# Optimization experiments

Measured on AMD Instinct MI355X. Metric: run time of the kernel, lower is better.

Reference implementation:

```python
import jax, jax.numpy as jnp
import numpy as np

B, N = 1024, 1024
OBS, ACT, WIDTH = 32, 8, 512

def setup_inputs() -> dict:
    key = jax.random.key(0)
    ks = jax.random.split(key, 8)
    s = 0.02  # small weight scale so 1024 Euler steps stay numerically stable
    return {
        "init_obs": jax.random.normal(ks[0], (B, OBS), jnp.float32),
        "actions": jax.random.normal(ks[1], (B, N, ACT), jnp.float32),
        "W0": jax.random.normal(ks[2], (WIDTH, OBS + ACT), jnp.float32) * s,
        "b0": jnp.zeros((WIDTH,), jnp.float32),
        "W1": jax.random.normal(ks[3], (WIDTH, WIDTH), jnp.float32) * s,
        "b1": jnp.zeros((WIDTH,), jnp.float32),
        "W2": jax.random.normal(ks[4], (WIDTH, WIDTH), jnp.float32) * s,
        "b2": jnp.zeros((WIDTH,), jnp.float32),
        "W3": jax.random.normal(ks[5], (OBS, WIDTH), jnp.float32) * s,
        "b3": jnp.zeros((OBS,), jnp.float32),
        "tau": 1,
    }

def _mlp(x, W0, b0, W1, b1, W2, b2, W3, b3):
    # eqx.nn.MLP with depth=3, activation=leaky_relu (no final activation)
    h = jax.nn.leaky_relu(x @ W0.T + b0)
    h = jax.nn.leaky_relu(h @ W1.T + b1)
    h = jax.nn.leaky_relu(h @ W2.T + b2)
    return h @ W3.T + b3

def reference(init_obs, actions, W0, b0, W1, b1, W2, b2, W3, b3, tau):
    # Fixed-step Euler integration: at step k (t = k*tau), action index = k.
    tauf = jnp.asarray(tau, init_obs.dtype)
    a_t = jnp.swapaxes(actions, 0, 1)  # (N, B, ACT)

    def step(y, a):
        dy = _mlp(jnp.concatenate([y, a], axis=-1), W0, b0, W1, b1, W2, b2, W3, b3)
        y_new = y + tauf * dy
        return y_new, y_new

    _, ys = jax.lax.scan(step, init_obs, a_t)  # ys: (N, B, OBS)
    traj = jnp.concatenate([init_obs[None], ys], axis=0)  # (N+1, B, OBS)
    return jnp.swapaxes(traj, 0, 1)  # (B, N+1, OBS)
```

## Files before the change

kernel.cpp:

```cpp
#include <hip/hip_runtime.h>
#include <hip/hip_bf16.h>
#include <stdint.h>

typedef __bf16 bf16;
typedef __attribute__((ext_vector_type(8))) __bf16 bf16x8;
typedef __attribute__((ext_vector_type(4))) float f32x4;
typedef __attribute__((ext_vector_type(2))) unsigned int u32x2;

#define MFMA_B16(a,b,c) __builtin_amdgcn_mfma_f32_16x16x32_bf16((a),(b),(c),0,0,0)

#define BATCH  1024
#define NSTEPS 1024
#define OBS    32
#define ACTD   8
#define WIDTH  512
#define ROWS   16
#define OUTS   ((NSTEPS+1)*OBS)
#define K0     128

#define W0P_OFF 0
#define W0P_N   (WIDTH*K0)
#define W1_OFF  (W0P_OFF + W0P_N)
#define WBIG_N  (WIDTH*WIDTH)
#define W2_OFF  (W1_OFF + WBIG_N)
#define W3_OFF  (W2_OFF + WBIG_N)
#define W3_N    (OBS*WIDTH)
#define TAU_OFF (W3_OFF + W3_N)
#define MB_OFF  606720
#define MB_N    (64*3*4*2048)
#define FLAG_DW_IDX (((MB_OFF + MB_N)/2) + 64)
#define NFLAG   (64*3*4*16)

#define LBAR() do{ asm volatile("s_waitcnt lgkmcnt(0)" ::: "memory"); \
                   __builtin_amdgcn_s_barrier(); \
                   __builtin_amdgcn_sched_barrier(0); }while(0)
#define FBAR() do{ asm volatile("s_waitcnt vmcnt(0) lgkmcnt(0)" ::: "memory"); \
                   __builtin_amdgcn_s_barrier(); \
                   __builtin_amdgcn_sched_barrier(0); }while(0)

__global__ void setup_kernel(const float* __restrict__ W0, const float* __restrict__ b0r,
                             const float* __restrict__ W1, const float* __restrict__ W2,
                             const float* __restrict__ W3,
                             const int* __restrict__ tau, bf16* __restrict__ wsb){
  int i = blockIdx.x*blockDim.x + threadIdx.x;
  int stride = gridDim.x*blockDim.x;
  for (int idx=i; idx<W0P_N; idx+=stride){
    int r = idx >> 7, c = idx & 127;
    float v = 0.0f;
    if (c < 32)       v = W0[r*40 + c];
    else if (c < 64)  v = W0[r*40 + (c-32)];
    else if (c < 72)  v = W0[r*40 + 32 + (c-64)];
    else if (c == 72) v = b0r[r];
    wsb[W0P_OFF+idx] = (bf16)v;
  }
  for (int idx=i; idx<WBIG_N; idx+=stride) wsb[W1_OFF+idx] = (bf16)W1[idx];
  for (int idx=i; idx<WBIG_N; idx+=stride) wsb[W2_OFF+idx] = (bf16)W2[idx];
  for (int idx=i; idx<W3_N;  idx+=stride) wsb[W3_OFF+idx] = (bf16)W3[idx];
  int* flags = ((int*)wsb) + FLAG_DW_IDX;
  for (int idx=i; idx<NFLAG; idx+=stride) flags[idx] = 0;
  if (i==0){
    int ti = *tau;
    float tf;
    if (ti >= -1000000 && ti <= 1000000) tf = (float)ti;
    else { union {int q; float f;} u; u.q = ti; tf = u.f; }
    *(float*)(wsb + TAU_OFF) = tf;
  }
}

__device__ __forceinline__ float leaky(float v){ return v < 0.0f ? 0.01f*v : v; }

__device__ __forceinline__ uint32_t pk2(float a, float b){
  union { bf16 h; uint16_t u; } ua, ub; ua.h = (bf16)a; ub.h = (bf16)b;
  return (uint32_t)ua.u | ((uint32_t)ub.u << 16);
}

__global__ __launch_bounds__(512, 2)
void ode_kernel(const float* __restrict__ init_obs, const float* __restrict__ actions,
                const float* __restrict__ b1g, const float* __restrict__ b2g,
                const float* __restrict__ b3g,
                bf16* __restrict__ wsrw, float* __restrict__ out){
  const bf16* w0g = wsrw + W0P_OFF;
  const bf16* w1g = wsrw + W1_OFF;
  const bf16* w2g = wsrw + W2_OFF;
  const bf16* w3g = wsrw + W3_OFF;
  unsigned long long* mbq = (unsigned long long*)(wsrw + MB_OFF);
  float* mbf = (float*)(wsrw + MB_OFF);
  int* flags = ((int*)wsrw) + FLAG_DW_IDX;
  const float tauf = *(const float*)(wsrw + TAU_OFF);

  __shared__ alignas(16) bf16 w0s[96*512];
  __shared__ alignas(16) bf16 w3s[8*512];
  __shared__ alignas(16) bf16 hF0[ROWS*WIDTH];
  __shared__ alignas(16) bf16 hF1[ROWS*WIDTH];
  __shared__ alignas(16) bf16 xin[ROWS*K0];
  __shared__ alignas(16) float pr[8][16][20];
  __shared__ float yS[ROWS][OBS];
  __shared__ int sdead;

  const int t    = threadIdx.x;
  const int lane = t & 63;
  const int wave = t >> 6;
  const int fm   = lane & 15;
  const int fk   = lane >> 4;
  const int b    = blockIdx.x;
  const int xcd  = b & 7, slot = b >> 3;
  const int g    = xcd*8 + (slot >> 2);
  const int j    = slot & 3;
  const int gb0  = g * ROWS;
  const int pm0 = (j==0)?1:0, pm1 = (j<2)?2:1, pm2 = (j<3)?3:2;

  const int hbase1 = fm*WIDTH + ((fk*8) ^ (fm*8));
  const int xbase0 = fm*K0    + ((fk*8) ^ (fm*8));
  const int chi    = j*128 + wave*16 + fk*4;

  const f32x4 b1q = *(const f32x4*)&b1g[chi];
  const f32x4 b2q = *(const f32x4*)&b2g[chi];

  bf16x8 w1f[16], w2f[16];
  {
    const bf16* p1 = w1g + (size_t)(j*128 + wave*16 + fm)*WIDTH + fk*8;
    const bf16* p2 = w2g + (size_t)(j*128 + wave*16 + fm)*WIDTH + fk*8;
    #pragma unroll
    for (int kk=0; kk<16; kk++) w1f[kk] = *(const bf16x8*)(p1 + kk*32);
    #pragma unroll
    for (int kk=0; kk<16; kk++) w2f[kk] = *(const bf16x8*)(p2 + kk*32);
  }
  {
    #pragma unroll
    for (int n=0; n<4; n++){
      const bf16* s0 = w0g + (size_t)((wave*4+n)*16 + fm)*K0 + fk*8;
      #pragma unroll
      for (int k=0; k<3; k++){
        bf16x8 v = *(const bf16x8*)(s0 + k*32);
        *(bf16x8*)&w0s[((wave*4+n)*3 + k)*512 + lane*8] = v;
      }
    }
    const int nt_ = wave & 1, q_ = wave >> 1;
    bf16x8 v3 = *(const bf16x8*)(w3g + (size_t)(nt_*16 + fm)*WIDTH + j*128 + q_*32 + fk*8);
    *(bf16x8*)&w3s[wave*512 + lane*8] = v3;
  }

  const int urow = t >> 5, ucol = t & 31;
  const float b3v = b3g[ucol];
  float* const outp = out + (size_t)(gb0 + urow)*OUTS + ucol;
  const int arow = (t >> 3) & 15, acol = t & 7;
  const float* const actp = actions + (size_t)(gb0 + arow)*(NSTEPS*ACTD) + acol;
  const int swU    = (urow & 15) << 3;
  const int xin_yh = urow*K0 + (ucol ^ swU);
  const int xin_yl = urow*K0 + ((ucol + 32) ^ swU);
  const int xin_ac = arow*K0 + ((64 + acol) ^ ((arow & 15) << 3));

  {
    if (t == 0) sdead = 0;
    #pragma unroll
    for (int q=0; q<(ROWS*K0)/512; q++) xin[q*512 + t] = (bf16)0.0f;
    __syncthreads();
    float yv = init_obs[(gb0 + urow)*OBS + ucol];
    yS[urow][ucol] = yv;
    if (j == 0) outp[0] = yv;
    bf16 yh = (bf16)yv;
    xin[xin_yh] = yh;
    xin[xin_yl] = (bf16)(yv - (float)yh);
    if (t < 128) xin[xin_ac] = (bf16)actp[0];
    if (t < 16)  xin[t*K0 + (72 ^ ((t&15)*8))] = (bf16)1.0f;
  }
  __syncthreads();

  #pragma unroll
  for (int kk=0; kk<16; kk++){ asm volatile("" : "+v"(w1f[kk])); }
  #pragma unroll
  for (int kk=0; kk<16; kk++){ asm volatile("" : "+v"(w2f[kk])); }

  #define STORE_OWN01(ACC, BQ, HF, HOP) do{ \
    float r0_ = leaky((ACC)[0] + (BQ)[0]); \
    float r1_ = leaky((ACC)[1] + (BQ)[1]); \
    float r2_ = leaky((ACC)[2] + (BQ)[2]); \
    float r3_ = leaky((ACC)[3] + (BQ)[3]); \
    union { u32x2 v; unsigned long long q; } pu_; \
    pu_.v = (u32x2){ pk2(r0_, r1_), pk2(r2_, r3_) }; \
    *(u32x2*)&HF[fm*WIDTH + (chi ^ (fm*8))] = pu_.v; \
    __hip_atomic_store(mbq + (size_t)((g*3+(HOP))*4 + j)*512 + fm*32 + wave*4 + fk, \
                       pu_.q, __ATOMIC_RELAXED, __HIP_MEMORY_SCOPE_AGENT); \
  }while(0)

  #define SYNC_HOP(HOP, ST1) do{ \
    FBAR(); \
    if (t == 0) __hip_atomic_store(flags + ((g*3+(HOP))*4 + j)*16, (ST1), \
                                   __ATOMIC_RELAXED, __HIP_MEMORY_SCOPE_AGENT); \
    if (wave == 0 && lane < 3){ \
      int pm_ = (lane==0)?pm0:((lane==1)?pm1:pm2); \
      const int* fp_ = flags + ((g*3+(HOP))*4 + pm_)*16; \
      int cnt_ = 0; \
      while (!*(volatile int*)&sdead && \
             __hip_atomic_load(fp_, __ATOMIC_RELAXED, __HIP_MEMORY_SCOPE_AGENT) < (ST1)){ \
        __builtin_amdgcn_s_sleep(1); \
        if (++cnt_ > (1<<20)) { *(volatile int*)&sdead = 1; break; } \
      } \
    } \
    LBAR(); \
  }while(0)

  #define GATHER01(HOP, DST) do{ \
    const int br_ = t >> 5, cg_ = t & 31; \
    const size_t hb_ = (size_t)((g*3+(HOP))*4); \
    unsigned long long v0_ = __hip_atomic_load(mbq + (hb_+pm0)*512 + br_*32 + cg_, \
                                 __ATOMIC_RELAXED, __HIP_MEMORY_SCOPE_AGENT); \
    unsigned long long v1_ = __hip_atomic_load(mbq + (hb_+pm1)*512 + br_*32 + cg_, \
                                 __ATOMIC_RELAXED, __HIP_MEMORY_SCOPE_AGENT); \
    unsigned long long v2_ = __hip_atomic_load(mbq + (hb_+pm2)*512 + br_*32 + cg_, \
                                 __ATOMIC_RELAXED, __HIP_MEMORY_SCOPE_AGENT); \
    *(unsigned long long*)&DST[br_*WIDTH + ((pm0*128 + cg_*4) ^ (br_*8))] = v0_; \
    *(unsigned long long*)&DST[br_*WIDTH + ((pm1*128 + cg_*4) ^ (br_*8))] = v1_; \
    *(unsigned long long*)&DST[br_*WIDTH + ((pm2*128 + cg_*4) ^ (br_*8))] = v2_; \
    LBAR(); \
  }while(0)

  #define L2Q(Q) do{ \
    _Pragma("unroll") \
    for (int kk=(Q)*4; kk<(Q)*4+4; kk++){ \
      bf16x8 bb = *(const bf16x8*)&hF1[hbase1 ^ (kk*32)]; \
      acc2 = MFMA_B16(w2f[kk], bb, acc2); \
    } \
  }while(0)

  #define L2MID() do{ \
    if (wave == 0 && lane < 3){ \
      int pm_ = (lane==0)?pm0:((lane==1)?pm1:pm2); \
      const int* fp_ = flags + ((g*3+0)*4 + pm_)*16; \
      int cnt_ = 0; \
      while (!*(volatile int*)&sdead && \
             __hip_atomic_load(fp_, __ATOMIC_RELAXED, __HIP_MEMORY_SCOPE_AGENT) < st1){ \
        __builtin_amdgcn_s_sleep(1); \
        if (++cnt_ > (1<<20)) { *(volatile int*)&sdead = 1; break; } \
      } \
    } \
    LBAR(); \
    GATHER01(0, hF1); \
  }while(0)

  const f32x4 z4 = {0,0,0,0};

  for (int s=0; s<NSTEPS; ++s){
    const int st1 = s + 1;
    const int sidx = (st1 < NSTEPS) ? st1 : 0;
    float av = actp[(size_t)sidx*ACTD];

    {
      #pragma unroll
      for (int n=0; n<4; n++){
        f32x4 acc = {0,0,0,0};
        #pragma unroll
        for (int k=0; k<3; k++){
          bf16x8 a  = *(const bf16x8*)&w0s[((wave*4+n)*3 + k)*512 + lane*8];
          bf16x8 bb = *(const bf16x8*)&xin[xbase0 ^ (k*32)];
          acc = MFMA_B16(a, bb, acc);
        }
        int ob = (wave*4+n)*16 + fk*4;
        u32x2 pw = { pk2(leaky(acc[0]), leaky(acc[1])),
                     pk2(leaky(acc[2]), leaky(acc[3])) };
        *(u32x2*)&hF0[fm*WIDTH + (ob ^ (fm*8))] = pw;
      }
    }
    LBAR();

    {
      f32x4 acc = {0,0,0,0};
      #pragma unroll
      for (int kk=0; kk<16; kk++){
        bf16x8 bb = *(const bf16x8*)&hF0[hbase1 ^ (kk*32)];
        acc = MFMA_B16(w1f[kk], bb, acc);
      }
      STORE_OWN01(acc, b1q, hF1, 0);
    }
    FBAR();
    if (t == 0) __hip_atomic_store(flags + ((g*3+0)*4 + j)*16, st1,
                                   __ATOMIC_RELAXED, __HIP_MEMORY_SCOPE_AGENT);

    f32x4 acc2 = {0,0,0,0};
    switch (j){
      case 0:  L2Q(0); L2MID(); L2Q(1); L2Q(2); L2Q(3); break;
      case 1:  L2Q(1); L2MID(); L2Q(0); L2Q(2); L2Q(3); break;
      case 2:  L2Q(2); L2MID(); L2Q(0); L2Q(1); L2Q(3); break;
      default: L2Q(3); L2MID(); L2Q(0); L2Q(1); L2Q(2); break;
    }
    {
      u32x2 pw = { pk2(leaky(acc2[0]+b2q[0]), leaky(acc2[1]+b2q[1])),
                   pk2(leaky(acc2[2]+b2q[2]), leaky(acc2[3]+b2q[3])) };
      *(u32x2*)&hF0[fm*WIDTH + (chi ^ (fm*8))] = pw;
    }
    LBAR();

    {
      const int q_ = wave >> 1;
      bf16x8 a  = *(const bf16x8*)&w3s[wave*512 + lane*8];
      bf16x8 bb = *(const bf16x8*)&hF0[fm*WIDTH + ((j*128 + q_*32 + fk*8) ^ (fm*8))];
      f32x4 a3 = MFMA_B16(a, bb, z4);
      *(f32x4*)&pr[wave][fm][fk*4] = a3;
    }
    LBAR();

    float ownv;
    {
      if (t < 128) xin[xin_ac] = (bf16)av;
      const int ntc = ucol >> 4, c15 = ucol & 15;
      ownv = ((pr[ntc][urow][c15] + pr[2+ntc][urow][c15])
              + pr[4+ntc][urow][c15]) + pr[6+ntc][urow][c15];
      __hip_atomic_store(mbf + (size_t)((g*3+2)*4 + j)*1024 + urow*32 + ucol,
                         ownv, __ATOMIC_RELAXED, __HIP_MEMORY_SCOPE_AGENT);
    }
    SYNC_HOP(2, st1);

    {
      float vals[4];
      #pragma unroll
      for (int m=0; m<4; m++){
        if (m == j) vals[m] = ownv;
        else vals[m] = __hip_atomic_load(mbf + (size_t)((g*3+2)*4 + m)*1024 + urow*32 + ucol,
                                         __ATOMIC_RELAXED, __HIP_MEMORY_SCOPE_AGENT);
      }
      float dy = b3v + vals[0] + vals[1] + vals[2] + vals[3];
      float yn = yS[urow][ucol] + tauf * dy;
      yS[urow][ucol] = yn;
      if (j == 0) outp[(size_t)st1*OBS] = yn;
      bf16 yh = (bf16)yn;
      xin[xin_yh] = yh;
      xin[xin_yl] = (bf16)(yn - (float)yh);
    }
    LBAR();
  }
  asm volatile("s_waitcnt vmcnt(0) lgkmcnt(0)" ::: "memory");
}

extern "C" void kernel_launch(void* const* d_in, const int* in_sizes, int n_in,
                              void* d_out, int out_size, void* d_ws, size_t ws_size,
                              hipStream_t stream){
  const float* init_obs = (const float*)d_in[0];
  const float* actions  = (const float*)d_in[1];
  const float* W0 = (const float*)d_in[2];
  const float* b0 = (const float*)d_in[3];
  const float* W1 = (const float*)d_in[4];
  const float* b1 = (const float*)d_in[5];
  const float* W2 = (const float*)d_in[6];
  const float* b2 = (const float*)d_in[7];
  const float* W3 = (const float*)d_in[8];
  const float* b3 = (const float*)d_in[9];
  const int*  tau = (const int*)d_in[10];
  bf16* wsb = (bf16*)d_ws;
  float* out = (float*)d_out;

  hipLaunchKernelGGL(setup_kernel, dim3(512), dim3(256), 0, stream,
                     W0, b0, W1, W2, W3, tau, wsb);
  hipLaunchKernelGGL(ode_kernel, dim3(256), dim3(512), 0, stream,
                     init_obs, actions, b1, b2, b3, wsb, out);
}
```

Before: 4.629 ms.

## Replace flag-based inter-block sync with step-tagged mailbox values polled per thread

Removes the separate flag arrays and the full-barrier-then-flag handshake between the four cooperating blocks. Each exchanged value now carries the step number in its upper 32 bits, so consumers poll the data words directly until the tags match. This drops a vmcnt-draining barrier and a flag round trip per hop, which should cut cross-block latency. In exchange each payload doubles in size, every thread spins on global loads, and the mailbox region must be zeroed in setup.

```diff
diff --git a/kernel.cpp b/kernel.cpp
--- a/kernel.cpp
+++ b/kernel.cpp
@@ -6,6 +6,7 @@
 typedef __attribute__((ext_vector_type(8))) __bf16 bf16x8;
 typedef __attribute__((ext_vector_type(4))) float f32x4;
 typedef __attribute__((ext_vector_type(2))) unsigned int u32x2;
+typedef unsigned long long u64;
 
 #define MFMA_B16(a,b,c) __builtin_amdgcn_mfma_f32_16x16x32_bf16((a),(b),(c),0,0,0)
 
@@ -26,15 +27,14 @@
 #define W3_OFF  (W2_OFF + WBIG_N)
 #define W3_N    (OBS*WIDTH)
 #define TAU_OFF (W3_OFF + W3_N)
-#define MB_OFF  606720
-#define MB_N    (64*3*4*2048)
-#define FLAG_DW_IDX (((MB_OFF + MB_N)/2) + 64)
-#define NFLAG   (64*3*4*16)
+#define MB_OFF      606720
+#define DY_U64_BASE 262144
+#define MB_U64_N    393216
+
+#define AL(P)   __hip_atomic_load((P),  __ATOMIC_RELAXED, __HIP_MEMORY_SCOPE_AGENT)
+#define AS(P,V) __hip_atomic_store((P), (V), __ATOMIC_RELAXED, __HIP_MEMORY_SCOPE_AGENT)
 
 #define LBAR() do{ asm volatile("s_waitcnt lgkmcnt(0)" ::: "memory"); \
-                   __builtin_amdgcn_s_barrier(); \
-                   __builtin_amdgcn_sched_barrier(0); }while(0)
-#define FBAR() do{ asm volatile("s_waitcnt vmcnt(0) lgkmcnt(0)" ::: "memory"); \
                    __builtin_amdgcn_s_barrier(); \
                    __builtin_amdgcn_sched_barrier(0); }while(0)
 
@@ -56,8 +56,8 @@
   for (int idx=i; idx<WBIG_N; idx+=stride) wsb[W1_OFF+idx] = (bf16)W1[idx];
   for (int idx=i; idx<WBIG_N; idx+=stride) wsb[W2_OFF+idx] = (bf16)W2[idx];
   for (int idx=i; idx<W3_N;  idx+=stride) wsb[W3_OFF+idx] = (bf16)W3[idx];
-  int* flags = ((int*)wsb) + FLAG_DW_IDX;
-  for (int idx=i; idx<NFLAG; idx+=stride) flags[idx] = 0;
+  u64* mbq = (u64*)(wsb + MB_OFF);
+  for (int idx=i; idx<MB_U64_N; idx+=stride) mbq[idx] = 0ull;
   if (i==0){
     int ti = *tau;
     float tf;
@@ -83,9 +83,7 @@
   const bf16* w1g = wsrw + W1_OFF;
   const bf16* w2g = wsrw + W2_OFF;
   const bf16* w3g = wsrw + W3_OFF;
-  unsigned long long* mbq = (unsigned long long*)(wsrw + MB_OFF);
-  float* mbf = (float*)(wsrw + MB_OFF);
-  int* flags = ((int*)wsrw) + FLAG_DW_IDX;
+  u64* mbq = (u64*)(wsrw + MB_OFF);
   const float tauf = *(const float*)(wsrw + TAU_OFF);
 
   __shared__ alignas(16) bf16 w0s[96*512];
@@ -171,71 +169,12 @@
   #pragma unroll
   for (int kk=0; kk<16; kk++){ asm volatile("" : "+v"(w2f[kk])); }
 
-  #define STORE_OWN01(ACC, BQ, HF, HOP) do{ \
-    float r0_ = leaky((ACC)[0] + (BQ)[0]); \
-    float r1_ = leaky((ACC)[1] + (BQ)[1]); \
-    float r2_ = leaky((ACC)[2] + (BQ)[2]); \
-    float r3_ = leaky((ACC)[3] + (BQ)[3]); \
-    union { u32x2 v; unsigned long long q; } pu_; \
-    pu_.v = (u32x2){ pk2(r0_, r1_), pk2(r2_, r3_) }; \
-    *(u32x2*)&HF[fm*WIDTH + (chi ^ (fm*8))] = pu_.v; \
-    __hip_atomic_store(mbq + (size_t)((g*3+(HOP))*4 + j)*512 + fm*32 + wave*4 + fk, \
-                       pu_.q, __ATOMIC_RELAXED, __HIP_MEMORY_SCOPE_AGENT); \
-  }while(0)
-
-  #define SYNC_HOP(HOP, ST1) do{ \
-    FBAR(); \
-    if (t == 0) __hip_atomic_store(flags + ((g*3+(HOP))*4 + j)*16, (ST1), \
-                                   __ATOMIC_RELAXED, __HIP_MEMORY_SCOPE_AGENT); \
-    if (wave == 0 && lane < 3){ \
-      int pm_ = (lane==0)?pm0:((lane==1)?pm1:pm2); \
-      const int* fp_ = flags + ((g*3+(HOP))*4 + pm_)*16; \
-      int cnt_ = 0; \
-      while (!*(volatile int*)&sdead && \
-             __hip_atomic_load(fp_, __ATOMIC_RELAXED, __HIP_MEMORY_SCOPE_AGENT) < (ST1)){ \
-        __builtin_amdgcn_s_sleep(1); \
-        if (++cnt_ > (1<<20)) { *(volatile int*)&sdead = 1; break; } \
-      } \
-    } \
-    LBAR(); \
-  }while(0)
-
-  #define GATHER01(HOP, DST) do{ \
-    const int br_ = t >> 5, cg_ = t & 31; \
-    const size_t hb_ = (size_t)((g*3+(HOP))*4); \
-    unsigned long long v0_ = __hip_atomic_load(mbq + (hb_+pm0)*512 + br_*32 + cg_, \
-                                 __ATOMIC_RELAXED, __HIP_MEMORY_SCOPE_AGENT); \
-    unsigned long long v1_ = __hip_atomic_load(mbq + (hb_+pm1)*512 + br_*32 + cg_, \
-                                 __ATOMIC_RELAXED, __HIP_MEMORY_SCOPE_AGENT); \
-    unsigned long long v2_ = __hip_atomic_load(mbq + (hb_+pm2)*512 + br_*32 + cg_, \
-                                 __ATOMIC_RELAXED, __HIP_MEMORY_SCOPE_AGENT); \
-    *(unsigned long long*)&DST[br_*WIDTH + ((pm0*128 + cg_*4) ^ (br_*8))] = v0_; \
-    *(unsigned long long*)&DST[br_*WIDTH + ((pm1*128 + cg_*4) ^ (br_*8))] = v1_; \
-    *(unsigned long long*)&DST[br_*WIDTH + ((pm2*128 + cg_*4) ^ (br_*8))] = v2_; \
-    LBAR(); \
-  }while(0)
-
   #define L2Q(Q) do{ \
     _Pragma("unroll") \
     for (int kk=(Q)*4; kk<(Q)*4+4; kk++){ \
-      bf16x8 bb = *(const bf16x8*)&hF1[hbase1 ^ (kk*32)]; \
-      acc2 = MFMA_B16(w2f[kk], bb, acc2); \
+      bf16x8 bb_ = *(const bf16x8*)&hF1[hbase1 ^ (kk*32)]; \
+      acc2 = MFMA_B16(w2f[kk], bb_, acc2); \
     } \
-  }while(0)
-
-  #define L2MID() do{ \
-    if (wave == 0 && lane < 3){ \
-      int pm_ = (lane==0)?pm0:((lane==1)?pm1:pm2); \
-      const int* fp_ = flags + ((g*3+0)*4 + pm_)*16; \
-      int cnt_ = 0; \
-      while (!*(volatile int*)&sdead && \
-             __hip_atomic_load(fp_, __ATOMIC_RELAXED, __HIP_MEMORY_SCOPE_AGENT) < st1){ \
-        __builtin_amdgcn_s_sleep(1); \
-        if (++cnt_ > (1<<20)) { *(volatile int*)&sdead = 1; break; } \
-      } \
-    } \
-    LBAR(); \
-    GATHER01(0, hF1); \
   }while(0)
 
   const f32x4 z4 = {0,0,0,0};
@@ -270,19 +209,51 @@
         bf16x8 bb = *(const bf16x8*)&hF0[hbase1 ^ (kk*32)];
         acc = MFMA_B16(w1f[kk], bb, acc);
       }
-      STORE_OWN01(acc, b1q, hF1, 0);
-    }
-    FBAR();
-    if (t == 0) __hip_atomic_store(flags + ((g*3+0)*4 + j)*16, st1,
-                                   __ATOMIC_RELAXED, __HIP_MEMORY_SCOPE_AGENT);
+      unsigned lo0 = pk2(leaky(acc[0]+b1q[0]), leaky(acc[1]+b1q[1]));
+      unsigned lo1 = pk2(leaky(acc[2]+b1q[2]), leaky(acc[3]+b1q[3]));
+      *(u64*)&hF1[fm*WIDTH + (chi ^ (fm*8))] = (u64)lo0 | ((u64)lo1 << 32);
+      u64 tg = ((u64)(unsigned)st1) << 32;
+      size_t mb = (size_t)(g*4 + j)*1024 + (size_t)(fm*32 + wave*4 + fk)*2;
+      AS(mbq + mb,     (u64)lo0 | tg);
+      AS(mbq + mb + 1, (u64)lo1 | tg);
+    }
+    LBAR();
 
     f32x4 acc2 = {0,0,0,0};
+    {
+      const int br = t >> 5, cg = t & 31;
+      const size_t hb = (size_t)(g*4);
+      const size_t ia = (hb+pm0)*1024 + (size_t)(br*32+cg)*2;
+      const size_t ib = (hb+pm1)*1024 + (size_t)(br*32+cg)*2;
+      const size_t ic = (hb+pm2)*1024 + (size_t)(br*32+cg)*2;
+      u64 a0 = AL(mbq+ia), a1 = AL(mbq+ia+1);
+      u64 b0 = AL(mbq+ib), b1 = AL(mbq+ib+1);
+      u64 c0 = AL(mbq+ic), c1 = AL(mbq+ic+1);
+      switch (j){ case 0: L2Q(0); break; case 1: L2Q(1); break;
+                  case 2: L2Q(2); break; default: L2Q(3); break; }
+      const unsigned sU = (unsigned)st1;
+      int cnt = 0;
+      while (!(((unsigned)(a0>>32)==sU) & ((unsigned)(a1>>32)==sU) &
+               ((unsigned)(b0>>32)==sU) & ((unsigned)(b1>>32)==sU) &
+               ((unsigned)(c0>>32)==sU) & ((unsigned)(c1>>32)==sU))){
+        if (*(volatile int*)&sdead) break;
+        __builtin_amdgcn_s_sleep(2);
+        if (++cnt > (1<<16)) { *(volatile int*)&sdead = 1; break; }
+        a0 = AL(mbq+ia); a1 = AL(mbq+ia+1);
+        b0 = AL(mbq+ib); b1 = AL(mbq+ib+1);
+        c0 = AL(mbq+ic); c1 = AL(mbq+ic+1);
+      }
+      const int sw = br << 3;
+      *(u64*)&hF1[br*WIDTH + ((pm0*128 + cg*4) ^ sw)] = (u64)(unsigned)a0 | ((u64)(unsigned)a1 << 32);
+      *(u64*)&hF1[br*WIDTH + ((pm1*128 + cg*4) ^ sw)] = (u64)(unsigned)b0 | ((u64)(unsigned)b1 << 32);
+      *(u64*)&hF1[br*WIDTH + ((pm2*128 + cg*4) ^ sw)] = (u64)(unsigned)c0 | ((u64)(unsigned)c1 << 32);
+    }
+    LBAR();
     switch (j){
-      case 0:  L2Q(0); L2MID(); L2Q(1); L2Q(2); L2Q(3); break;
-      case 1:  L2Q(1); L2MID(); L2Q(0); L2Q(2); L2Q(3); break;
-      case 2:  L2Q(2); L2MID(); L2Q(0); L2Q(1); L2Q(3); break;
-      default: L2Q(3); L2MID(); L2Q(0); L2Q(1); L2Q(2); break;
-    }
+      case 0:  L2Q(1); L2Q(2); L2Q(3); break;
+      case 1:  L2Q(0); L2Q(2); L2Q(3); break;
+      case 2:  L2Q(0); L2Q(1); L2Q(3); break;
+      default: L2Q(0); L2Q(1); L2Q(2); break; }
     {
       u32x2 pw = { pk2(leaky(acc2[0]+b2q[0]), leaky(acc2[1]+b2q[1])),
                    pk2(leaky(acc2[2]+b2q[2]), leaky(acc2[3]+b2q[3])) };
@@ -305,20 +276,34 @@
       const int ntc = ucol >> 4, c15 = ucol & 15;
       ownv = ((pr[ntc][urow][c15] + pr[2+ntc][urow][c15])
               + pr[4+ntc][urow][c15]) + pr[6+ntc][urow][c15];
-      __hip_atomic_store(mbf + (size_t)((g*3+2)*4 + j)*1024 + urow*32 + ucol,
-                         ownv, __ATOMIC_RELAXED, __HIP_MEMORY_SCOPE_AGENT);
-    }
-    SYNC_HOP(2, st1);
-
-    {
-      float vals[4];
-      #pragma unroll
-      for (int m=0; m<4; m++){
-        if (m == j) vals[m] = ownv;
-        else vals[m] = __hip_atomic_load(mbf + (size_t)((g*3+2)*4 + m)*1024 + urow*32 + ucol,
-                                         __ATOMIC_RELAXED, __HIP_MEMORY_SCOPE_AGENT);
-      }
-      float dy = b3v + vals[0] + vals[1] + vals[2] + vals[3];
+      AS(mbq + DY_U64_BASE + (size_t)(g*4 + j)*512 + urow*32 + ucol,
+         (u64)__float_as_uint(ownv) | (((u64)(unsigned)st1) << 32));
+    }
+
+    {
+      const size_t db = DY_U64_BASE + (size_t)(g*4)*512 + (size_t)(urow*32 + ucol);
+      u64 va = AL(mbq + db + (size_t)pm0*512);
+      u64 vb = AL(mbq + db + (size_t)pm1*512);
+      u64 vc = AL(mbq + db + (size_t)pm2*512);
+      const unsigned sU = (unsigned)st1;
+      int cnt = 0;
+      while (!(((unsigned)(va>>32)==sU) & ((unsigned)(vb>>32)==sU) &
+               ((unsigned)(vc>>32)==sU))){
+        if (*(volatile int*)&sdead) break;
+        __builtin_amdgcn_s_sleep(2);
+        if (++cnt > (1<<16)) { *(volatile int*)&sdead = 1; break; }
+        va = AL(mbq + db + (size_t)pm0*512);
+        vb = AL(mbq + db + (size_t)pm1*512);
+        vc = AL(mbq + db + (size_t)pm2*512);
+      }
+      float v0 = __uint_as_float((unsigned)va);
+      float v1 = __uint_as_float((unsigned)vb);
+      float v2 = __uint_as_float((unsigned)vc);
+      float a0 = (j==0) ? ownv : v0;
+      float a1 = (j==1) ? ownv : ((j==0) ? v0 : v1);
+      float a2 = (j==2) ? ownv : ((j<2) ? v1 : v2);
+      float a3 = (j==3) ? ownv : v2;
+      float dy = b3v + a0 + a1 + a2 + a3;
       float yn = yS[urow][ucol] + tauf * dy;
       yS[urow][ucol] = yn;
       if (j == 0) outp[(size_t)st1*OBS] = yn;
```

New measurement: 7.822 ms. 1.69x slower.
